# Performance work log

Hardware: AMD Instinct MI355X
Metric: run time of the kernel (lower is better)

## Reference

```python
import jax, jax.numpy as jnp
import numpy as np

N, D = 100000, 64        # num nodes, node feature dim
E, DE = 1600000, 64      # num edges, edge feature dim
MSG_H, MSG_OUT = 128, 64 # message MLP hidden sizes (activate_final=True)
NODE_H = 128             # node MLP hidden; final size = D (residual)
LN_EPS = 1e-5


def setup_inputs() -> dict:
    key = jax.random.key(0)
    ks = jax.random.split(key, 10)
    def glorot(k, shape):
        fan_in = shape[0]
        return jax.random.normal(k, shape, jnp.float32) / jnp.sqrt(jnp.float32(fan_in))
    return {
        "nodes": jax.random.normal(ks[0], (N, D), jnp.float32),
        "edges": jax.random.normal(ks[1], (E, DE), jnp.float32),
        "senders": jax.random.randint(ks[2], (E,), 0, N, jnp.int32),
        "receivers": jax.random.randint(ks[3], (E,), 0, N, jnp.int32),
        "msg_W1": glorot(ks[4], (2 * D + DE, MSG_H)),
        "msg_b1": jnp.zeros((MSG_H,), jnp.float32),
        "msg_W2": glorot(ks[5], (MSG_H, MSG_OUT)),
        "msg_b2": jnp.zeros((MSG_OUT,), jnp.float32),
        "node_W1": glorot(ks[6], (D + MSG_OUT, NODE_H)),
        "node_b1": jnp.zeros((NODE_H,), jnp.float32),
        "node_W2": glorot(ks[7], (NODE_H, D)),
        "node_b2": jnp.zeros((D,), jnp.float32),
        "ln_scale": jnp.ones((D,), jnp.float32),
        "ln_offset": jnp.zeros((D,), jnp.float32),
    }


def reference(nodes, edges, senders, receivers,
              msg_W1, msg_b1, msg_W2, msg_b2,
              node_W1, node_b1, node_W2, node_b2,
              ln_scale, ln_offset):
    # --- message MLP (activate_final=True) over concat(sender, receiver, edge)
    x = jnp.concatenate([nodes[senders], nodes[receivers], edges], axis=-1)  # [E, 2D+DE]
    h = jax.nn.relu(x @ msg_W1 + msg_b1)
    messages = jax.nn.relu(h @ msg_W2 + msg_b2)  # [E, MSG_OUT]
    # --- aggregate messages at receivers
    agg = jax.ops.segment_sum(messages, receivers, num_segments=nodes.shape[0])  # [N, MSG_OUT]
    # --- node update MLP (no final activation), sizes [NODE_H, D] due to residual
    y = jnp.concatenate([nodes, agg], axis=-1)  # [N, D+MSG_OUT]
    y = jax.nn.relu(y @ node_W1 + node_b1)
    y = y @ node_W2 + node_b2  # [N, D]
    # --- layer norm over last axis with scale + offset
    mean = jnp.mean(y, axis=-1, keepdims=True)
    var = jnp.var(y, axis=-1, keepdims=True)
    y = (y - mean) * jax.lax.rsqrt(var + LN_EPS) * ln_scale + ln_offset
    # --- residual connection
    return nodes + y
```

## Files before the change

### kernel.cpp

```cpp
#include <hip/hip_runtime.h>

typedef short bf16x8 __attribute__((ext_vector_type(8)));
typedef float floatx4 __attribute__((ext_vector_type(4)));
typedef unsigned short u16x4 __attribute__((ext_vector_type(4)));
typedef unsigned short u16x8 __attribute__((ext_vector_type(8)));

__device__ __forceinline__ unsigned short f2bf(float f) {
  union { float f; unsigned int u; } v;
  v.f = f;
  unsigned int u = v.u + (0x7FFFu + ((v.u >> 16) & 1u));
  return (unsigned short)(u >> 16);
}

__global__ __launch_bounds__(256) void prep_weights(
    const float* __restrict__ mW1, const float* __restrict__ mW2,
    const float* __restrict__ nW1, const float* __restrict__ nW2,
    unsigned short* __restrict__ W1f, unsigned short* __restrict__ W2f,
    unsigned short* __restrict__ NW1f, unsigned short* __restrict__ NW2f) {
  int idx = blockIdx.x * 256 + threadIdx.x;
  if (idx < 24576) {
    int j = idx & 7, n = (idx >> 3) & 127, g = idx >> 10;
    W1f[idx] = f2bf(mW1[(g * 8 + j) * 128 + n]);
  } else if (idx < 32768) {
    int t = idx - 24576;
    int j = t & 7, n = (t >> 3) & 63, g = t >> 9;
    W2f[t] = f2bf(mW2[(g * 8 + j) * 64 + n]);
  } else if (idx < 49152) {
    int t = idx - 32768;
    int j = t & 7, n = (t >> 3) & 127, g = t >> 10;
    NW1f[t] = f2bf(nW1[(g * 8 + j) * 128 + n]);
  } else if (idx < 57344) {
    int t = idx - 49152;
    int j = t & 7, n = (t >> 3) & 63, g = t >> 9;
    NW2f[t] = f2bf(nW2[(g * 8 + j) * 64 + n]);
  }
}

__global__ __launch_bounds__(256) void edge_kernel(
    const float* __restrict__ nodes, const float* __restrict__ edges,
    const int* __restrict__ senders, const int* __restrict__ receivers,
    const unsigned short* __restrict__ W1f, const unsigned short* __restrict__ W2f,
    const float* __restrict__ b1, const float* __restrict__ b2,
    float* agg, int E) {
  __shared__ int snd[128];
  __shared__ int rcv[128];
  __shared__ unsigned short Xs[128 * 40];
  __shared__ unsigned short Ws[4096];
  __shared__ unsigned short Hl[128 * 136];

  const int tid = threadIdx.x;
  const int e0 = blockIdx.x * 128;
  const int w = tid >> 6, lane = tid & 63;
  const int col = lane & 15, quad = lane >> 4;
  const int wm = w & 1, wn = w >> 1;

  if (tid < 128) {
    int ge = e0 + tid;
    snd[tid] = (ge < E) ? senders[ge] : 0;
    rcv[tid] = (ge < E) ? receivers[ge] : 0;
  }

  floatx4 z4 = {0.f, 0.f, 0.f, 0.f};
  floatx4 acc1[4][4];
#pragma unroll
  for (int mt = 0; mt < 4; ++mt)
#pragma unroll
    for (int nt = 0; nt < 4; ++nt) acc1[mt][nt] = z4;

  for (int ks = 0; ks < 6; ++ks) {
    __syncthreads();
    for (int t = tid; t < 1024; t += 256) {
      int e = t >> 3, c = t & 7;
      float4 v;
      if (e0 + e < E) {
        int off = (ks & 1) * 32 + c * 4;
        const float* src;
        if (ks < 2)      src = nodes + (size_t)snd[e] * 64 + off;
        else if (ks < 4) src = nodes + (size_t)rcv[e] * 64 + off;
        else             src = edges + (size_t)(e0 + e) * 64 + off;
        v = *(const float4*)src;
      } else {
        v = make_float4(0.f, 0.f, 0.f, 0.f);
      }
      u16x4 h;
      h.x = f2bf(v.x); h.y = f2bf(v.y); h.z = f2bf(v.z); h.w = f2bf(v.w);
      *(u16x4*)&Xs[e * 40 + c * 4] = h;
    }
    *(u16x8*)&Ws[tid * 8] = *(const u16x8*)&W1f[ks * 4096 + tid * 8];
    *(u16x8*)&Ws[(tid + 256) * 8] = *(const u16x8*)&W1f[ks * 4096 + (tid + 256) * 8];
    __syncthreads();

    bf16x8 a[4], b[4];
#pragma unroll
    for (int mt = 0; mt < 4; ++mt)
      a[mt] = *(const bf16x8*)&Xs[(wm * 64 + mt * 16 + col) * 40 + quad * 8];
#pragma unroll
    for (int nt = 0; nt < 4; ++nt)
      b[nt] = *(const bf16x8*)&Ws[(quad * 128 + wn * 64 + nt * 16 + col) * 8];
#pragma unroll
    for (int mt = 0; mt < 4; ++mt)
#pragma unroll
      for (int nt = 0; nt < 4; ++nt)
        acc1[mt][nt] = __builtin_amdgcn_mfma_f32_16x16x32_bf16(a[mt], b[nt], acc1[mt][nt], 0, 0, 0);
  }

#pragma unroll
  for (int nt = 0; nt < 4; ++nt) {
    float bias = b1[wn * 64 + nt * 16 + col];
#pragma unroll
    for (int mt = 0; mt < 4; ++mt)
#pragma unroll
      for (int r = 0; r < 4; ++r) {
        float v = acc1[mt][nt][r] + bias;
        v = v > 0.f ? v : 0.f;
        Hl[(wm * 64 + mt * 16 + quad * 4 + r) * 136 + wn * 64 + nt * 16 + col] = f2bf(v);
      }
  }

  floatx4 acc2[4][2];
#pragma unroll
  for (int mt = 0; mt < 4; ++mt) { acc2[mt][0] = z4; acc2[mt][1] = z4; }

  for (int ks = 0; ks < 4; ++ks) {
    __syncthreads();
    *(u16x8*)&Ws[tid * 8] = *(const u16x8*)&W2f[ks * 2048 + tid * 8];
    __syncthreads();
    bf16x8 a[4], b[2];
#pragma unroll
    for (int mt = 0; mt < 4; ++mt)
      a[mt] = *(const bf16x8*)&Hl[(wm * 64 + mt * 16 + col) * 136 + ks * 32 + quad * 8];
#pragma unroll
    for (int nt = 0; nt < 2; ++nt)
      b[nt] = *(const bf16x8*)&Ws[(quad * 64 + wn * 32 + nt * 16 + col) * 8];
#pragma unroll
    for (int mt = 0; mt < 4; ++mt)
#pragma unroll
      for (int nt = 0; nt < 2; ++nt)
        acc2[mt][nt] = __builtin_amdgcn_mfma_f32_16x16x32_bf16(a[mt], b[nt], acc2[mt][nt], 0, 0, 0);
  }

  float bs0 = b2[wn * 32 + col];
  float bs1 = b2[wn * 32 + 16 + col];
#pragma unroll
  for (int mt = 0; mt < 4; ++mt)
#pragma unroll
    for (int r = 0; r < 4; ++r) {
      int i = wm * 64 + mt * 16 + quad * 4 + r;
      if (e0 + i < E) {
        int rv = rcv[i];
        float v0 = acc2[mt][0][r] + bs0; v0 = v0 > 0.f ? v0 : 0.f;
        float v1 = acc2[mt][1][r] + bs1; v1 = v1 > 0.f ? v1 : 0.f;
        atomicAdd(&agg[(size_t)rv * 64 + wn * 32 + col], v0);
        atomicAdd(&agg[(size_t)rv * 64 + wn * 32 + 16 + col], v1);
      }
    }
}

__global__ __launch_bounds__(256) void node_kernel(
    const float* __restrict__ nodes, const float* agg,
    const unsigned short* __restrict__ W1f, const unsigned short* __restrict__ W2f,
    const float* __restrict__ b1, const float* __restrict__ b2,
    const float* __restrict__ ln_s, const float* __restrict__ ln_o,
    float* out, int N) {
  __shared__ unsigned short Xs[128 * 40];
  __shared__ unsigned short Ws[4096];
  __shared__ unsigned short Hl[128 * 136];
  __shared__ float Ls1[128][2];
  __shared__ float Ls2[128][2];

  const int tid = threadIdx.x;
  const int n0 = blockIdx.x * 128;
  const int w = tid >> 6, lane = tid & 63;
  const int col = lane & 15, quad = lane >> 4;
  const int wm = w & 1, wn = w >> 1;

  floatx4 z4 = {0.f, 0.f, 0.f, 0.f};
  floatx4 acc1[4][4];
#pragma unroll
  for (int mt = 0; mt < 4; ++mt)
#pragma unroll
    for (int nt = 0; nt < 4; ++nt) acc1[mt][nt] = z4;

  for (int ks = 0; ks < 4; ++ks) {
    __syncthreads();
    for (int t = tid; t < 1024; t += 256) {
      int e = t >> 3, c = t & 7;
      int gi = n0 + e;
      float4 v;
      if (gi < N) {
        const float* src = ((ks < 2) ? nodes : agg) + (size_t)gi * 64 + (ks & 1) * 32 + c * 4;
        v = *(const float4*)src;
      } else {
        v = make_float4(0.f, 0.f, 0.f, 0.f);
      }
      u16x4 h;
      h.x = f2bf(v.x); h.y = f2bf(v.y); h.z = f2bf(v.z); h.w = f2bf(v.w);
      *(u16x4*)&Xs[e * 40 + c * 4] = h;
    }
    *(u16x8*)&Ws[tid * 8] = *(const u16x8*)&W1f[ks * 4096 + tid * 8];
    *(u16x8*)&Ws[(tid + 256) * 8] = *(const u16x8*)&W1f[ks * 4096 + (tid + 256) * 8];
    __syncthreads();

    bf16x8 a[4], b[4];
#pragma unroll
    for (int mt = 0; mt < 4; ++mt)
      a[mt] = *(const bf16x8*)&Xs[(wm * 64 + mt * 16 + col) * 40 + quad * 8];
#pragma unroll
    for (int nt = 0; nt < 4; ++nt)
      b[nt] = *(const bf16x8*)&Ws[(quad * 128 + wn * 64 + nt * 16 + col) * 8];
#pragma unroll
    for (int mt = 0; mt < 4; ++mt)
#pragma unroll
      for (int nt = 0; nt < 4; ++nt)
        acc1[mt][nt] = __builtin_amdgcn_mfma_f32_16x16x32_bf16(a[mt], b[nt], acc1[mt][nt], 0, 0, 0);
  }

#pragma unroll
  for (int nt = 0; nt < 4; ++nt) {
    float bias = b1[wn * 64 + nt * 16 + col];
#pragma unroll
    for (int mt = 0; mt < 4; ++mt)
#pragma unroll
      for (int r = 0; r < 4; ++r) {
        float v = acc1[mt][nt][r] + bias;
        v = v > 0.f ? v : 0.f;
        Hl[(wm * 64 + mt * 16 + quad * 4 + r) * 136 + wn * 64 + nt * 16 + col] = f2bf(v);
      }
  }

  floatx4 acc2[4][2];
#pragma unroll
  for (int mt = 0; mt < 4; ++mt) { acc2[mt][0] = z4; acc2[mt][1] = z4; }

  for (int ks = 0; ks < 4; ++ks) {
    __syncthreads();
    *(u16x8*)&Ws[tid * 8] = *(const u16x8*)&W2f[ks * 2048 + tid * 8];
    __syncthreads();
    bf16x8 a[4], b[2];
#pragma unroll
    for (int mt = 0; mt < 4; ++mt)
      a[mt] = *(const bf16x8*)&Hl[(wm * 64 + mt * 16 + col) * 136 + ks * 32 + quad * 8];
#pragma unroll
    for (int nt = 0; nt < 2; ++nt)
      b[nt] = *(const bf16x8*)&Ws[(quad * 64 + wn * 32 + nt * 16 + col) * 8];
#pragma unroll
    for (int mt = 0; mt < 4; ++mt)
#pragma unroll
      for (int nt = 0; nt < 2; ++nt)
        acc2[mt][nt] = __builtin_amdgcn_mfma_f32_16x16x32_bf16(a[mt], b[nt], acc2[mt][nt], 0, 0, 0);
  }

  float y[4][2][4];
  float bs0 = b2[wn * 32 + col];
  float bs1 = b2[wn * 32 + 16 + col];
#pragma unroll
  for (int mt = 0; mt < 4; ++mt)
#pragma unroll
    for (int r = 0; r < 4; ++r) {
      y[mt][0][r] = acc2[mt][0][r] + bs0;
      y[mt][1][r] = acc2[mt][1][r] + bs1;
    }

#pragma unroll
  for (int mt = 0; mt < 4; ++mt)
#pragma unroll
    for (int r = 0; r < 4; ++r) {
      float p1 = y[mt][0][r] + y[mt][1][r];
      float p2 = y[mt][0][r] * y[mt][0][r] + y[mt][1][r] * y[mt][1][r];
#pragma unroll
      for (int m = 1; m <= 8; m <<= 1) {
        p1 += __shfl_xor(p1, m);
        p2 += __shfl_xor(p2, m);
      }
      if (col == 0) {
        int row = wm * 64 + mt * 16 + quad * 4 + r;
        Ls1[row][wn] = p1;
        Ls2[row][wn] = p2;
      }
    }
  __syncthreads();

  float lsv0 = ln_s[wn * 32 + col],      lsv1 = ln_s[wn * 32 + 16 + col];
  float lov0 = ln_o[wn * 32 + col],      lov1 = ln_o[wn * 32 + 16 + col];
#pragma unroll
  for (int mt = 0; mt < 4; ++mt)
#pragma unroll
    for (int r = 0; r < 4; ++r) {
      int row = wm * 64 + mt * 16 + quad * 4 + r;
      int gi = n0 + row;
      float s1 = Ls1[row][0] + Ls1[row][1];
      float s2 = Ls2[row][0] + Ls2[row][1];
      float mean = s1 * (1.f / 64.f);
      float var = s2 * (1.f / 64.f) - mean * mean;
      float rstd = rsqrtf(var + 1e-5f);
      if (gi < N) {
        int j0 = wn * 32 + col;
        float o0 = (y[mt][0][r] - mean) * rstd * lsv0 + lov0 + nodes[(size_t)gi * 64 + j0];
        float o1 = (y[mt][1][r] - mean) * rstd * lsv1 + lov1 + nodes[(size_t)gi * 64 + j0 + 16];
        out[(size_t)gi * 64 + j0] = o0;
        out[(size_t)gi * 64 + j0 + 16] = o1;
      }
    }
}

extern "C" void kernel_launch(void* const* d_in, const int* in_sizes, int n_in,
                              void* d_out, int out_size, void* d_ws, size_t ws_size,
                              hipStream_t stream) {
  const float* nodes     = (const float*)d_in[0];
  const float* edges     = (const float*)d_in[1];
  const int*   senders   = (const int*)d_in[2];
  const int*   receivers = (const int*)d_in[3];
  const float* msg_W1    = (const float*)d_in[4];
  const float* msg_b1    = (const float*)d_in[5];
  const float* msg_W2    = (const float*)d_in[6];
  const float* msg_b2    = (const float*)d_in[7];
  const float* node_W1   = (const float*)d_in[8];
  const float* node_b1   = (const float*)d_in[9];
  const float* node_W2   = (const float*)d_in[10];
  const float* node_b2   = (const float*)d_in[11];
  const float* ln_scale  = (const float*)d_in[12];
  const float* ln_offset = (const float*)d_in[13];

  const int N = in_sizes[0] / 64;
  const int E = in_sizes[2];

  unsigned short* W1f  = (unsigned short*)d_ws;
  unsigned short* W2f  = W1f + 24576;
  unsigned short* NW1f = W2f + 8192;
  unsigned short* NW2f = NW1f + 16384;

  float* agg = (float*)d_out;

  hipMemsetAsync(d_out, 0, (size_t)out_size * sizeof(float), stream);
  prep_weights<<<224, 256, 0, stream>>>(msg_W1, msg_W2, node_W1, node_W2, W1f, W2f, NW1f, NW2f);
  edge_kernel<<<(E + 127) / 128, 256, 0, stream>>>(nodes, edges, senders, receivers,
                                                   W1f, W2f, msg_b1, msg_b2, agg, E);
  node_kernel<<<(N + 127) / 128, 256, 0, stream>>>(nodes, agg, NW1f, NW2f,
                                                   node_b1, node_b2, ln_scale, ln_offset,
                                                   (float*)d_out, N);
}
```

Baseline: 1.178 ms.

## Load MFMA operands directly from global memory with a bf16 node copy

Adds a pre-pass that converts node features to bf16 once. The edge and node kernels then load their MFMA A and B fragments straight from global memory (gathered bf16 rows, weights, edges converted in registers) instead of staging them through LDS with barriers between k-steps. This removes the per-k-step shared-memory staging and synchronisation, cuts LDS use and adds an occupancy hint of 3 blocks per CU. In exchange, weight fragments are re-read from global or L2 by every wave, each lane gathers uncoalesced 16-byte pieces, and the extra conversion kernel adds a launch and a write of the bf16 node copy.

```diff
diff --git a/kernel.cpp b/kernel.cpp
--- a/kernel.cpp
+++ b/kernel.cpp
@@ -10,6 +10,13 @@
   v.f = f;
   unsigned int u = v.u + (0x7FFFu + ((v.u >> 16) & 1u));
   return (unsigned short)(u >> 16);
+}
+
+__device__ __forceinline__ bf16x8 pack8(float4 a, float4 b) {
+  u16x8 h;
+  h[0] = f2bf(a.x); h[1] = f2bf(a.y); h[2] = f2bf(a.z); h[3] = f2bf(a.w);
+  h[4] = f2bf(b.x); h[5] = f2bf(b.y); h[6] = f2bf(b.z); h[7] = f2bf(b.w);
+  union { u16x8 u; bf16x8 s; } cv; cv.u = h; return cv.s;
 }
 
 __global__ __launch_bounds__(256) void prep_weights(
@@ -36,16 +43,22 @@
   }
 }
 
-__global__ __launch_bounds__(256) void edge_kernel(
-    const float* __restrict__ nodes, const float* __restrict__ edges,
+__global__ __launch_bounds__(256) void conv_nodes(
+    const float* __restrict__ nodes, unsigned short* __restrict__ nodes_bf, int total4) {
+  int i = (blockIdx.x * 256 + threadIdx.x) * 4;
+  if (i < total4) {
+    float4 v = *(const float4*)(nodes + i);
+    u16x4 h; h[0] = f2bf(v.x); h[1] = f2bf(v.y); h[2] = f2bf(v.z); h[3] = f2bf(v.w);
+    *(u16x4*)(nodes_bf + i) = h;
+  }
+}
+
+__global__ __launch_bounds__(256, 3) void edge_kernel(
+    const float* __restrict__ edges, const unsigned short* __restrict__ nodes_bf,
     const int* __restrict__ senders, const int* __restrict__ receivers,
     const unsigned short* __restrict__ W1f, const unsigned short* __restrict__ W2f,
     const float* __restrict__ b1, const float* __restrict__ b2,
     float* agg, int E) {
-  __shared__ int snd[128];
-  __shared__ int rcv[128];
-  __shared__ unsigned short Xs[128 * 40];
-  __shared__ unsigned short Ws[4096];
   __shared__ unsigned short Hl[128 * 136];
 
   const int tid = threadIdx.x;
@@ -54,11 +67,14 @@
   const int col = lane & 15, quad = lane >> 4;
   const int wm = w & 1, wn = w >> 1;
 
-  if (tid < 128) {
-    int ge = e0 + tid;
-    snd[tid] = (ge < E) ? senders[ge] : 0;
-    rcv[tid] = (ge < E) ? receivers[ge] : 0;
-  }
+  int srow[4], sndi[4], rcvi[4];
+#pragma unroll
+  for (int mt = 0; mt < 4; ++mt) {
+    int r = e0 + wm * 64 + mt * 16 + col;
+    srow[mt] = r < E ? r : E - 1;
+  }
+#pragma unroll
+  for (int mt = 0; mt < 4; ++mt) { sndi[mt] = senders[srow[mt]]; rcvi[mt] = receivers[srow[mt]]; }
 
   floatx4 z4 = {0.f, 0.f, 0.f, 0.f};
   floatx4 acc1[4][4];
@@ -67,36 +83,36 @@
 #pragma unroll
     for (int nt = 0; nt < 4; ++nt) acc1[mt][nt] = z4;
 
-  for (int ks = 0; ks < 6; ++ks) {
-    __syncthreads();
-    for (int t = tid; t < 1024; t += 256) {
-      int e = t >> 3, c = t & 7;
-      float4 v;
-      if (e0 + e < E) {
-        int off = (ks & 1) * 32 + c * 4;
-        const float* src;
-        if (ks < 2)      src = nodes + (size_t)snd[e] * 64 + off;
-        else if (ks < 4) src = nodes + (size_t)rcv[e] * 64 + off;
-        else             src = edges + (size_t)(e0 + e) * 64 + off;
-        v = *(const float4*)src;
-      } else {
-        v = make_float4(0.f, 0.f, 0.f, 0.f);
-      }
-      u16x4 h;
-      h.x = f2bf(v.x); h.y = f2bf(v.y); h.z = f2bf(v.z); h.w = f2bf(v.w);
-      *(u16x4*)&Xs[e * 40 + c * 4] = h;
-    }
-    *(u16x8*)&Ws[tid * 8] = *(const u16x8*)&W1f[ks * 4096 + tid * 8];
-    *(u16x8*)&Ws[(tid + 256) * 8] = *(const u16x8*)&W1f[ks * 4096 + (tid + 256) * 8];
-    __syncthreads();
-
+#pragma unroll
+  for (int ks = 0; ks < 4; ++ks) {
     bf16x8 a[4], b[4];
 #pragma unroll
-    for (int mt = 0; mt < 4; ++mt)
-      a[mt] = *(const bf16x8*)&Xs[(wm * 64 + mt * 16 + col) * 40 + quad * 8];
+    for (int mt = 0; mt < 4; ++mt) {
+      int nd = (ks < 2) ? sndi[mt] : rcvi[mt];
+      a[mt] = *(const bf16x8*)&nodes_bf[(size_t)nd * 64 + (ks & 1) * 32 + quad * 8];
+    }
 #pragma unroll
     for (int nt = 0; nt < 4; ++nt)
-      b[nt] = *(const bf16x8*)&Ws[(quad * 128 + wn * 64 + nt * 16 + col) * 8];
+      b[nt] = *(const bf16x8*)&W1f[ks * 4096 + quad * 1024 + (wn * 64 + nt * 16 + col) * 8];
+#pragma unroll
+    for (int mt = 0; mt < 4; ++mt)
+#pragma unroll
+      for (int nt = 0; nt < 4; ++nt)
+        acc1[mt][nt] = __builtin_amdgcn_mfma_f32_16x16x32_bf16(a[mt], b[nt], acc1[mt][nt], 0, 0, 0);
+  }
+#pragma unroll
+  for (int ks = 4; ks < 6; ++ks) {
+    bf16x8 a[4], b[4];
+#pragma unroll
+    for (int mt = 0; mt < 4; ++mt) {
+      const float* p = edges + (size_t)srow[mt] * 64 + (ks - 4) * 32 + quad * 8;
+      float4 v0 = *(const float4*)p;
+      float4 v1 = *(const float4*)(p + 4);
+      a[mt] = pack8(v0, v1);
+    }
+#pragma unroll
+    for (int nt = 0; nt < 4; ++nt)
+      b[nt] = *(const bf16x8*)&W1f[ks * 4096 + quad * 1024 + (wn * 64 + nt * 16 + col) * 8];
 #pragma unroll
     for (int mt = 0; mt < 4; ++mt)
 #pragma unroll
@@ -116,22 +132,21 @@
         Hl[(wm * 64 + mt * 16 + quad * 4 + r) * 136 + wn * 64 + nt * 16 + col] = f2bf(v);
       }
   }
+  __syncthreads();
 
   floatx4 acc2[4][2];
 #pragma unroll
   for (int mt = 0; mt < 4; ++mt) { acc2[mt][0] = z4; acc2[mt][1] = z4; }
 
+#pragma unroll
   for (int ks = 0; ks < 4; ++ks) {
-    __syncthreads();
-    *(u16x8*)&Ws[tid * 8] = *(const u16x8*)&W2f[ks * 2048 + tid * 8];
-    __syncthreads();
     bf16x8 a[4], b[2];
 #pragma unroll
     for (int mt = 0; mt < 4; ++mt)
       a[mt] = *(const bf16x8*)&Hl[(wm * 64 + mt * 16 + col) * 136 + ks * 32 + quad * 8];
 #pragma unroll
     for (int nt = 0; nt < 2; ++nt)
-      b[nt] = *(const bf16x8*)&Ws[(quad * 64 + wn * 32 + nt * 16 + col) * 8];
+      b[nt] = *(const bf16x8*)&W2f[ks * 2048 + quad * 512 + (wn * 32 + nt * 16 + col) * 8];
 #pragma unroll
     for (int mt = 0; mt < 4; ++mt)
 #pragma unroll
@@ -145,9 +160,9 @@
   for (int mt = 0; mt < 4; ++mt)
 #pragma unroll
     for (int r = 0; r < 4; ++r) {
-      int i = wm * 64 + mt * 16 + quad * 4 + r;
-      if (e0 + i < E) {
-        int rv = rcv[i];
+      int er = e0 + wm * 64 + mt * 16 + quad * 4 + r;
+      if (er < E) {
+        int rv = receivers[er];
         float v0 = acc2[mt][0][r] + bs0; v0 = v0 > 0.f ? v0 : 0.f;
         float v1 = acc2[mt][1][r] + bs1; v1 = v1 > 0.f ? v1 : 0.f;
         atomicAdd(&agg[(size_t)rv * 64 + wn * 32 + col], v0);
@@ -156,14 +171,13 @@
     }
 }
 
-__global__ __launch_bounds__(256) void node_kernel(
-    const float* __restrict__ nodes, const float* agg,
+__global__ __launch_bounds__(256, 3) void node_kernel(
+    const float* __restrict__ nodes, const unsigned short* __restrict__ nodes_bf,
+    const float* agg,
     const unsigned short* __restrict__ W1f, const unsigned short* __restrict__ W2f,
     const float* __restrict__ b1, const float* __restrict__ b2,
     const float* __restrict__ ln_s, const float* __restrict__ ln_o,
     float* out, int N) {
-  __shared__ unsigned short Xs[128 * 40];
-  __shared__ unsigned short Ws[4096];
   __shared__ unsigned short Hl[128 * 136];
   __shared__ float Ls1[128][2];
   __shared__ float Ls2[128][2];
@@ -174,6 +188,13 @@
   const int col = lane & 15, quad = lane >> 4;
   const int wm = w & 1, wn = w >> 1;
 
+  int arow[4];
+#pragma unroll
+  for (int mt = 0; mt < 4; ++mt) {
+    int r = n0 + wm * 64 + mt * 16 + col;
+    arow[mt] = r < N ? r : N - 1;
+  }
+
   floatx4 z4 = {0.f, 0.f, 0.f, 0.f};
   floatx4 acc1[4][4];
 #pragma unroll
@@ -181,33 +202,34 @@
 #pragma unroll
     for (int nt = 0; nt < 4; ++nt) acc1[mt][nt] = z4;
 
-  for (int ks = 0; ks < 4; ++ks) {
-    __syncthreads();
-    for (int t = tid; t < 1024; t += 256) {
-      int e = t >> 3, c = t & 7;
-      int gi = n0 + e;
-      float4 v;
-      if (gi < N) {
-        const float* src = ((ks < 2) ? nodes : agg) + (size_t)gi * 64 + (ks & 1) * 32 + c * 4;
-        v = *(const float4*)src;
-      } else {
-        v = make_float4(0.f, 0.f, 0.f, 0.f);
-      }
-      u16x4 h;
-      h.x = f2bf(v.x); h.y = f2bf(v.y); h.z = f2bf(v.z); h.w = f2bf(v.w);
-      *(u16x4*)&Xs[e * 40 + c * 4] = h;
-    }
-    *(u16x8*)&Ws[tid * 8] = *(const u16x8*)&W1f[ks * 4096 + tid * 8];
-    *(u16x8*)&Ws[(tid + 256) * 8] = *(const u16x8*)&W1f[ks * 4096 + (tid + 256) * 8];
-    __syncthreads();
-
+#pragma unroll
+  for (int ks = 0; ks < 2; ++ks) {
     bf16x8 a[4], b[4];
 #pragma unroll
     for (int mt = 0; mt < 4; ++mt)
-      a[mt] = *(const bf16x8*)&Xs[(wm * 64 + mt * 16 + col) * 40 + quad * 8];
+      a[mt] = *(const bf16x8*)&nodes_bf[(size_t)arow[mt] * 64 + ks * 32 + quad * 8];
 #pragma unroll
     for (int nt = 0; nt < 4; ++nt)
-      b[nt] = *(const bf16x8*)&Ws[(quad * 128 + wn * 64 + nt * 16 + col) * 8];
+      b[nt] = *(const bf16x8*)&W1f[ks * 4096 + quad * 1024 + (wn * 64 + nt * 16 + col) * 8];
+#pragma unroll
+    for (int mt = 0; mt < 4; ++mt)
+#pragma unroll
+      for (int nt = 0; nt < 4; ++nt)
+        acc1[mt][nt] = __builtin_amdgcn_mfma_f32_16x16x32_bf16(a[mt], b[nt], acc1[mt][nt], 0, 0, 0);
+  }
+#pragma unroll
+  for (int ks = 2; ks < 4; ++ks) {
+    bf16x8 a[4], b[4];
+#pragma unroll
+    for (int mt = 0; mt < 4; ++mt) {
+      const float* p = agg + (size_t)arow[mt] * 64 + (ks - 2) * 32 + quad * 8;
+      float4 v0 = *(const float4*)p;
+      float4 v1 = *(const float4*)(p + 4);
+      a[mt] = pack8(v0, v1);
+    }
+#pragma unroll
+    for (int nt = 0; nt < 4; ++nt)
+      b[nt] = *(const bf16x8*)&W1f[ks * 4096 + quad * 1024 + (wn * 64 + nt * 16 + col) * 8];
 #pragma unroll
     for (int mt = 0; mt < 4; ++mt)
 #pragma unroll
@@ -227,22 +249,21 @@
         Hl[(wm * 64 + mt * 16 + quad * 4 + r) * 136 + wn * 64 + nt * 16 + col] = f2bf(v);
       }
   }
+  __syncthreads();
 
   floatx4 acc2[4][2];
 #pragma unroll
   for (int mt = 0; mt < 4; ++mt) { acc2[mt][0] = z4; acc2[mt][1] = z4; }
 
+#pragma unroll
   for (int ks = 0; ks < 4; ++ks) {
-    __syncthreads();
-    *(u16x8*)&Ws[tid * 8] = *(const u16x8*)&W2f[ks * 2048 + tid * 8];
-    __syncthreads();
     bf16x8 a[4], b[2];
 #pragma unroll
     for (int mt = 0; mt < 4; ++mt)
       a[mt] = *(const bf16x8*)&Hl[(wm * 64 + mt * 16 + col) * 136 + ks * 32 + quad * 8];
 #pragma unroll
     for (int nt = 0; nt < 2; ++nt)
-      b[nt] = *(const bf16x8*)&Ws[(quad * 64 + wn * 32 + nt * 16 + col) * 8];
+      b[nt] = *(const bf16x8*)&W2f[ks * 2048 + quad * 512 + (wn * 32 + nt * 16 + col) * 8];
 #pragma unroll
     for (int mt = 0; mt < 4; ++mt)
 #pragma unroll
@@ -280,8 +301,8 @@
     }
   __syncthreads();
 
-  float lsv0 = ln_s[wn * 32 + col],      lsv1 = ln_s[wn * 32 + 16 + col];
-  float lov0 = ln_o[wn * 32 + col],      lov1 = ln_o[wn * 32 + 16 + col];
+  float lsv0 = ln_s[wn * 32 + col], lsv1 = ln_s[wn * 32 + 16 + col];
+  float lov0 = ln_o[wn * 32 + col], lov1 = ln_o[wn * 32 + 16 + col];
 #pragma unroll
   for (int mt = 0; mt < 4; ++mt)
 #pragma unroll
@@ -328,14 +349,16 @@
   unsigned short* W2f  = W1f + 24576;
   unsigned short* NW1f = W2f + 8192;
   unsigned short* NW2f = NW1f + 16384;
+  unsigned short* nodes_bf = NW2f + 8192;
 
   float* agg = (float*)d_out;
 
   hipMemsetAsync(d_out, 0, (size_t)out_size * sizeof(float), stream);
   prep_weights<<<224, 256, 0, stream>>>(msg_W1, msg_W2, node_W1, node_W2, W1f, W2f, NW1f, NW2f);
-  edge_kernel<<<(E + 127) / 128, 256, 0, stream>>>(nodes, edges, senders, receivers,
+  conv_nodes<<<(N * 64 + 1023) / 1024, 256, 0, stream>>>(nodes, nodes_bf, N * 64);
+  edge_kernel<<<(E + 127) / 128, 256, 0, stream>>>(edges, nodes_bf, senders, receivers,
                                                    W1f, W2f, msg_b1, msg_b2, agg, E);
-  node_kernel<<<(N + 127) / 128, 256, 0, stream>>>(nodes, agg, NW1f, NW2f,
+  node_kernel<<<(N + 127) / 128, 256, 0, stream>>>(nodes, nodes_bf, agg, NW1f, NW2f,
                                                    node_b1, node_b2, ln_scale, ln_offset,
                                                    (float*)d_out, N);
 }
```

After: 1.011 ms. -14.2%, faster.
